# Optimization experiments

Hardware: AMD Instinct MI355X
Metric: run time of the kernel (lower is better)

## Reference

```python
import jax, jax.numpy as jnp
import numpy as np

B, T, D, K = 8, 2048, 256, 8192
COMMITMENT_COST = 0.25

def setup_inputs() -> dict:
    key = jax.random.key(0)
    k1, k2 = jax.random.split(key)
    xs = jax.random.normal(k1, (B, T, D), dtype=jnp.float32)
    # lengths: all full so max(ilens) == T and the wrapper slice is a no-op (static shapes for jit)
    ilens = jnp.full((B,), T, dtype=jnp.int64)
    codebook = jax.random.normal(k2, (K, D), dtype=jnp.float32)
    return {"xs": xs, "ilens": ilens, "codebook": codebook}

def reference(xs, ilens, codebook):
    # Quantizer.forward: slice xs to max(ilens) (no-op here, max(ilens)==T),
    # then VectorQuantize: euclidean nearest-codebook search + commitment loss.
    x_sq = jnp.sum(xs * xs, axis=-1, keepdims=True)              # (B, T, 1)
    c_sq = jnp.sum(codebook * codebook, axis=-1)                 # (K,)
    dots = jnp.einsum('btd,kd->btk', xs, codebook)               # (B, T, K)
    dist = x_sq - 2.0 * dots + c_sq                              # (B, T, K)
    indices = jnp.argmin(dist, axis=-1)                          # (B, T)
    quantized = codebook[indices]                                # (B, T, D) gather
    # commitment loss: mse(quantize.detach(), x)
    diff = jax.lax.stop_gradient(quantized) - xs
    commit_loss = jnp.mean(diff * diff)
    loss = COMMITMENT_COST * commit_loss
    return (loss, commit_loss)
```

## Files before the change

kernel.cpp:

```cpp
#include <hip/hip_runtime.h>
#include <stdint.h>

#define M_TOK 16384
#define DIM   256
#define KCB   8192
#define NGRP  8
#define GRP   1024
#define NCHK  16
#define NT    16
#define SHIFT 512.0f
#define INV_N (1.0f / 4194304.0f)
#define SC1   0x7F7F7F7F

typedef __attribute__((ext_vector_type(4))) float f32x4;
typedef __attribute__((ext_vector_type(8))) int   i32x8;

static __device__ __forceinline__ void lds_cp16(const void* g, void* l) {
    __builtin_amdgcn_global_load_lds(
        (const __attribute__((address_space(1))) void*)g,
        (__attribute__((address_space(3))) void*)l, 16, 0, 0);
}

static __device__ __forceinline__ int pk4(float4 f) {
    int o = __builtin_amdgcn_cvt_pk_fp8_f32(f.x, f.y, 0, false);
    o     = __builtin_amdgcn_cvt_pk_fp8_f32(f.z, f.w, o, true);
    return o;
}

__global__ void k_prep(const float* __restrict__ cb,
                       unsigned char* __restrict__ cbt,
                       float* __restrict__ chalf) {
    __shared__ float part[4][64];
    const int w  = threadIdx.x >> 6;
    const int l  = threadIdx.x & 63;
    const int c0 = blockIdx.x * 64;
    const float* row = cb + (size_t)(c0 + l) * DIM;
    float s = 0.0f;
    #pragma unroll
    for (int j = 0; j < 4; j++) {
        int ch = w * 4 + j;
        const float* p = row + ch * 16;
        float4 a = *(const float4*)(p);
        float4 b = *(const float4*)(p + 4);
        float4 c = *(const float4*)(p + 8);
        float4 d = *(const float4*)(p + 12);
        s += a.x*a.x + a.y*a.y + a.z*a.z + a.w*a.w
           + b.x*b.x + b.y*b.y + b.z*b.z + b.w*b.w
           + c.x*c.x + c.y*c.y + c.z*c.z + c.w*c.w
           + d.x*d.x + d.y*d.y + d.z*d.z + d.w*d.w;
        float4 na = {-a.x, -a.y, -a.z, -a.w};
        float4 nb = {-b.x, -b.y, -b.z, -b.w};
        float4 nc = {-c.x, -c.y, -c.z, -c.w};
        float4 nd = {-d.x, -d.y, -d.z, -d.w};
        uint4 r;
        r.x = (unsigned)pk4(na); r.y = (unsigned)pk4(nb);
        r.z = (unsigned)pk4(nc); r.w = (unsigned)pk4(nd);
        *(uint4*)(cbt + ((size_t)ch * KCB + c0 + l) * 16) = r;
    }
    part[w][l] = s;
    __syncthreads();
    if (w == 0) {
        float t = part[0][l] + part[1][l] + part[2][l] + part[3][l];
        chalf[c0 + l] = 0.5f * t + SHIFT;
    }
}

__global__ __launch_bounds__(256, 4) void k_gemm_argmin(
    const float* __restrict__ xs,
    const unsigned char* __restrict__ cbt,
    const float* __restrict__ chalf,
    uint32_t* __restrict__ pkey)
{
    __shared__ __align__(16) unsigned char Bs[2][NCHK][64][16];
    __shared__ float schalf[GRP];

    const int tid  = threadIdx.x;
    const int w    = tid >> 6;
    const int l    = tid & 63;
    const int lrow = l & 15;
    const int quad = l >> 4;
    const int m0 = blockIdx.x * 128;
    const int g  = blockIdx.y;

    *(float4*)&schalf[tid * 4] = ((const float4*)(chalf + g * GRP))[tid];

    const unsigned char* bsrc = cbt + ((size_t)(w * 4) * KCB + g * GRP + l) * 16;

    #pragma unroll
    for (int j = 0; j < 4; j++)
        lds_cp16(bsrc + (size_t)j * KCB * 16, &Bs[0][w * 4 + j][0][0]);

    i32x8 afr[2][2];
    {
        const float* ap = xs + (size_t)(m0 + w * 32 + lrow) * DIM + quad * 32;
        #pragma unroll
        for (int rt = 0; rt < 2; rt++)
            #pragma unroll
            for (int ks = 0; ks < 2; ks++) {
                const float* p = ap + rt * 16 * DIM + ks * 128;
                union { int d[8]; i32x8 v; } aa;
                #pragma unroll
                for (int d = 0; d < 8; d++)
                    aa.d[d] = pk4(*(const float4*)(p + d * 4));
                afr[rt][ks] = aa.v;
            }
    }

    uint32_t best[2][4];
    #pragma unroll
    for (int rt = 0; rt < 2; rt++)
        #pragma unroll
        for (int rg = 0; rg < 4; rg++) best[rt][rg] = 0xFFFFFFFFu;

    #pragma unroll 1
    for (int t = 0; t < NT; t++) {
        const int cur = t & 1;
        __syncthreads();
        if (t < NT - 1) {
            #pragma unroll
            for (int j = 0; j < 4; j++)
                lds_cp16(bsrc + ((size_t)j * KCB + (t + 1) * 64) * 16,
                         &Bs[1 - cur][w * 4 + j][0][0]);
        }

        f32x4 acc[2][4];
        #pragma unroll
        for (int ct = 0; ct < 4; ct++) {
            float cs = schalf[t * 64 + ct * 16 + lrow];
            #pragma unroll
            for (int rt = 0; rt < 2; rt++) {
                f32x4 c4 = {cs, cs, cs, cs};
                acc[rt][ct] = c4;
            }
        }
        #pragma unroll
        for (int ks = 0; ks < 2; ks++) {
            const int ch = ks * 8 + quad * 2;
            i32x8 bfr[4];
            #pragma unroll
            for (int ct = 0; ct < 4; ct++) {
                union { uint4 q[2]; i32x8 v; } bb;
                bb.q[0] = *(const uint4*)&Bs[cur][ch][ct * 16 + lrow][0];
                bb.q[1] = *(const uint4*)&Bs[cur][ch + 1][ct * 16 + lrow][0];
                bfr[ct] = bb.v;
            }
            #pragma unroll
            for (int rt = 0; rt < 2; rt++)
                #pragma unroll
                for (int ct = 0; ct < 4; ct++)
                    acc[rt][ct] = __builtin_amdgcn_mfma_scale_f32_16x16x128_f8f6f4(
                        afr[rt][ks], bfr[ct], acc[rt][ct],
                        0, 0,
                        0, SC1,
                        0, SC1);
        }
        #pragma unroll
        for (int ct = 0; ct < 4; ct++) {
            uint32_t idl = (uint32_t)(t * 64 + ct * 16 + lrow);
            #pragma unroll
            for (int rt = 0; rt < 2; rt++)
                #pragma unroll
                for (int rg = 0; rg < 4; rg++) {
                    uint32_t key =
                        (__float_as_uint(acc[rt][ct][rg]) & 0xFFFFFC00u) | idl;
                    if (key < best[rt][rg]) best[rt][rg] = key;
                }
        }
    }

    #pragma unroll
    for (int off = 1; off < 16; off <<= 1)
        #pragma unroll
        for (int rt = 0; rt < 2; rt++)
            #pragma unroll
            for (int rg = 0; rg < 4; rg++) {
                uint32_t o = __shfl_xor(best[rt][rg], off);
                if (o < best[rt][rg]) best[rt][rg] = o;
            }
    if (lrow == 0) {
        #pragma unroll
        for (int rt = 0; rt < 2; rt++)
            #pragma unroll
            for (int rg = 0; rg < 4; rg++)
                pkey[(size_t)(m0 + w * 32 + rt * 16 + quad * 4 + rg) * NGRP + g]
                    = best[rt][rg];
    }
}

__global__ void k_finalize(const uint32_t* __restrict__ pkey,
                           const float4* __restrict__ xs4,
                           const float4* __restrict__ cb4,
                           float* __restrict__ partial) {
    __shared__ float sblk[4];
    int w   = threadIdx.x >> 6;
    int row = blockIdx.x * 4 + w;
    int l   = threadIdx.x & 63;
    uint32_t k = 0xFFFFFFFFu;
    int g = 0;
    if (l < 8) { k = pkey[(size_t)row * NGRP + l]; g = l; }
    #pragma unroll
    for (int off = 1; off < 8; off <<= 1) {
        uint32_t ok = __shfl_xor(k, off);
        int      og = __shfl_xor(g, off);
        if (ok < k) { k = ok; g = og; }
    }
    k = __shfl(k, 0);
    g = __shfl(g, 0);
    int code = g * GRP + (int)(k & 1023u);
    float4 x = xs4[(size_t)row * 64 + l];
    float4 c = cb4[(size_t)code * 64 + l];
    float dx = x.x - c.x, dy = x.y - c.y, dz = x.z - c.z, dw = x.w - c.w;
    float s = dx * dx + dy * dy + dz * dz + dw * dw;
    #pragma unroll
    for (int off = 32; off; off >>= 1) s += __shfl_xor(s, off);
    if (l == 0) sblk[w] = s;
    __syncthreads();
    if (threadIdx.x == 0)
        partial[blockIdx.x] = sblk[0] + sblk[1] + sblk[2] + sblk[3];
}

__global__ void k_write(const float* __restrict__ partial,
                        float* __restrict__ out) {
    __shared__ float swv[16];
    int tid = threadIdx.x;
    float s = partial[tid] + partial[tid + 1024] +
              partial[tid + 2048] + partial[tid + 3072];
    #pragma unroll
    for (int off = 32; off; off >>= 1) s += __shfl_xor(s, off);
    if ((tid & 63) == 0) swv[tid >> 6] = s;
    __syncthreads();
    if (tid == 0) {
        float t = 0.0f;
        #pragma unroll
        for (int i = 0; i < 16; i++) t += swv[i];
        float commit = t * INV_N;
        out[0] = 0.25f * commit;
        out[1] = commit;
    }
}

extern "C" void kernel_launch(void* const* d_in, const int* in_sizes, int n_in,
                              void* d_out, int out_size, void* d_ws, size_t ws_size,
                              hipStream_t stream) {
    const float* xs = (const float*)d_in[0];
    const float* cb = (const float*)d_in[2];

    char* ws = (char*)d_ws;
    unsigned char* cbt     = (unsigned char*)(ws + 256);
    float*         chalf   = (float*)(ws + 256 + 2097152);
    uint32_t*      pkey    = (uint32_t*)(ws + 256 + 2129920);
    float*         partial = (float*)(ws + 256 + 2654208);

    k_prep<<<128, 256, 0, stream>>>(cb, cbt, chalf);
    dim3 g(M_TOK / 128, NGRP);
    k_gemm_argmin<<<g, 256, 0, stream>>>(xs, cbt, chalf, pkey);
    k_finalize<<<4096, 256, 0, stream>>>(pkey, (const float4*)xs,
                                         (const float4*)cb, partial);
    k_write<<<1, 1024, 0, stream>>>(partial, (float*)d_out);
}
```

Measured before the change: 119.6 us.

## Prefetch two stages ahead with explicit waitcnt and barrier scheduling in GEMM-argmin

The codebook tile pipeline in the fused GEMM/argmin kernel becomes prefetch-distance two. Two tiles are issued up front, and the loop uses explicit vmcnt waits, raw s_barrier and sched_barrier, and setprio around the MFMA bursts. The next load is issued mid-iteration, after the second k-slice's B fragments are read into registers, so the previous global load latency can overlap compute. The prep kernel is also split over twice as many blocks, each handling 32 codes, to raise parallelism. The hand-placed waitcnts are fragile and rely on the exact count of outstanding loads.

```diff
diff --git a/kernel.cpp b/kernel.cpp
--- a/kernel.cpp
+++ b/kernel.cpp
@@ -30,15 +30,18 @@
 __global__ void k_prep(const float* __restrict__ cb,
                        unsigned char* __restrict__ cbt,
                        float* __restrict__ chalf) {
-    __shared__ float part[4][64];
-    const int w  = threadIdx.x >> 6;
-    const int l  = threadIdx.x & 63;
-    const int c0 = blockIdx.x * 64;
-    const float* row = cb + (size_t)(c0 + l) * DIM;
+    __shared__ float part[8][32];
+    const int w    = threadIdx.x >> 6;
+    const int l    = threadIdx.x & 63;
+    const int code = l & 31;
+    const int sub  = l >> 5;
+    const int grp8 = w * 2 + sub;
+    const int c0   = blockIdx.x * 32;
+    const float* row = cb + (size_t)(c0 + code) * DIM;
     float s = 0.0f;
     #pragma unroll
-    for (int j = 0; j < 4; j++) {
-        int ch = w * 4 + j;
+    for (int j = 0; j < 2; j++) {
+        int ch = grp8 * 2 + j;
         const float* p = row + ch * 16;
         float4 a = *(const float4*)(p);
         float4 b = *(const float4*)(p + 4);
@@ -55,12 +58,14 @@
         uint4 r;
         r.x = (unsigned)pk4(na); r.y = (unsigned)pk4(nb);
         r.z = (unsigned)pk4(nc); r.w = (unsigned)pk4(nd);
-        *(uint4*)(cbt + ((size_t)ch * KCB + c0 + l) * 16) = r;
-    }
-    part[w][l] = s;
+        *(uint4*)(cbt + ((size_t)ch * KCB + c0 + code) * 16) = r;
+    }
+    part[grp8][code] = s;
     __syncthreads();
-    if (w == 0) {
-        float t = part[0][l] + part[1][l] + part[2][l] + part[3][l];
+    if (w == 0 && l < 32) {
+        float t = 0.0f;
+        #pragma unroll
+        for (int i = 0; i < 8; i++) t += part[i][l];
         chalf[c0 + l] = 0.5f * t + SHIFT;
     }
 }
@@ -82,13 +87,7 @@
     const int m0 = blockIdx.x * 128;
     const int g  = blockIdx.y;
 
-    *(float4*)&schalf[tid * 4] = ((const float4*)(chalf + g * GRP))[tid];
-
     const unsigned char* bsrc = cbt + ((size_t)(w * 4) * KCB + g * GRP + l) * 16;
-
-    #pragma unroll
-    for (int j = 0; j < 4; j++)
-        lds_cp16(bsrc + (size_t)j * KCB * 16, &Bs[0][w * 4 + j][0][0]);
 
     i32x8 afr[2][2];
     {
@@ -106,6 +105,16 @@
             }
     }
 
+    *(float4*)&schalf[tid * 4] = ((const float4*)(chalf + g * GRP))[tid];
+    asm volatile("s_waitcnt lgkmcnt(0)" ::: "memory");
+
+    #pragma unroll
+    for (int j = 0; j < 4; j++)
+        lds_cp16(bsrc + ((size_t)j * KCB + 0 * 64) * 16, &Bs[0][w * 4 + j][0][0]);
+    #pragma unroll
+    for (int j = 0; j < 4; j++)
+        lds_cp16(bsrc + ((size_t)j * KCB + 1 * 64) * 16, &Bs[1][w * 4 + j][0][0]);
+
     uint32_t best[2][4];
     #pragma unroll
     for (int rt = 0; rt < 2; rt++)
@@ -115,13 +124,10 @@
     #pragma unroll 1
     for (int t = 0; t < NT; t++) {
         const int cur = t & 1;
-        __syncthreads();
-        if (t < NT - 1) {
-            #pragma unroll
-            for (int j = 0; j < 4; j++)
-                lds_cp16(bsrc + ((size_t)j * KCB + (t + 1) * 64) * 16,
-                         &Bs[1 - cur][w * 4 + j][0][0]);
-        }
+        if (t == NT - 1) asm volatile("s_waitcnt vmcnt(0)" ::: "memory");
+        else             asm volatile("s_waitcnt vmcnt(4)" ::: "memory");
+        __builtin_amdgcn_s_barrier();
+        __builtin_amdgcn_sched_barrier(0);
 
         f32x4 acc[2][4];
         #pragma unroll
@@ -133,9 +139,9 @@
                 acc[rt][ct] = c4;
             }
         }
-        #pragma unroll
-        for (int ks = 0; ks < 2; ks++) {
-            const int ch = ks * 8 + quad * 2;
+
+        {
+            const int ch = quad * 2;
             i32x8 bfr[4];
             #pragma unroll
             for (int ct = 0; ct < 4; ct++) {
@@ -144,16 +150,50 @@
                 bb.q[1] = *(const uint4*)&Bs[cur][ch + 1][ct * 16 + lrow][0];
                 bfr[ct] = bb.v;
             }
+            __builtin_amdgcn_s_setprio(1);
             #pragma unroll
             for (int rt = 0; rt < 2; rt++)
                 #pragma unroll
                 for (int ct = 0; ct < 4; ct++)
                     acc[rt][ct] = __builtin_amdgcn_mfma_scale_f32_16x16x128_f8f6f4(
-                        afr[rt][ks], bfr[ct], acc[rt][ct],
-                        0, 0,
-                        0, SC1,
-                        0, SC1);
-        }
+                        afr[rt][0], bfr[ct], acc[rt][ct],
+                        0, 0, 0, SC1, 0, SC1);
+            __builtin_amdgcn_s_setprio(0);
+        }
+
+        i32x8 bfr1[4];
+        {
+            const int ch = 8 + quad * 2;
+            #pragma unroll
+            for (int ct = 0; ct < 4; ct++) {
+                union { uint4 q[2]; i32x8 v; } bb;
+                bb.q[0] = *(const uint4*)&Bs[cur][ch][ct * 16 + lrow][0];
+                bb.q[1] = *(const uint4*)&Bs[cur][ch + 1][ct * 16 + lrow][0];
+                bfr1[ct] = bb.v;
+            }
+        }
+        asm volatile("s_waitcnt lgkmcnt(0)" ::: "memory");
+        __builtin_amdgcn_sched_barrier(0);
+        __builtin_amdgcn_s_barrier();
+        __builtin_amdgcn_sched_barrier(0);
+
+        if (t < NT - 2) {
+            #pragma unroll
+            for (int j = 0; j < 4; j++)
+                lds_cp16(bsrc + ((size_t)j * KCB + (t + 2) * 64) * 16,
+                         &Bs[cur][w * 4 + j][0][0]);
+        }
+
+        __builtin_amdgcn_s_setprio(1);
+        #pragma unroll
+        for (int rt = 0; rt < 2; rt++)
+            #pragma unroll
+            for (int ct = 0; ct < 4; ct++)
+                acc[rt][ct] = __builtin_amdgcn_mfma_scale_f32_16x16x128_f8f6f4(
+                    afr[rt][1], bfr1[ct], acc[rt][ct],
+                    0, 0, 0, SC1, 0, SC1);
+        __builtin_amdgcn_s_setprio(0);
+
         #pragma unroll
         for (int ct = 0; ct < 4; ct++) {
             uint32_t idl = (uint32_t)(t * 64 + ct * 16 + lrow);
@@ -251,7 +291,7 @@
     uint32_t*      pkey    = (uint32_t*)(ws + 256 + 2129920);
     float*         partial = (float*)(ws + 256 + 2654208);
 
-    k_prep<<<128, 256, 0, stream>>>(cb, cbt, chalf);
+    k_prep<<<256, 256, 0, stream>>>(cb, cbt, chalf);
     dim3 g(M_TOK / 128, NGRP);
     k_gemm_argmin<<<g, 256, 0, stream>>>(xs, cbt, chalf, pkey);
     k_finalize<<<4096, 256, 0, stream>>>(pkey, (const float4*)xs,
```

After: 158.8 us. +32.9%, slower.

## Keep codebook fragments in registers and stream pre-quantized fp8 activations

Applied to the files above, without the earlier changes.

Before, each block held a 128-row activation tile in registers and streamed 1024 codes through LDS. Now each wave keeps a 64-code slice of the fp8 codebook in registers and streams 512 rows of activations, which k_prep pre-quantizes to fp8 in a chunked layout. Each wave reduces one 16-row step across its 64 codes, writing 128 partial keys per row instead of 8. k_finalize reduces those keys and also does the final sum via an atomic last-block counter, removing the separate k_write launch. The trade is many more partial-key writes and reads plus an extra activation quantization pass, in exchange for dropping LDS staging and barriers.

```diff
diff --git a/kernel.cpp b/kernel.cpp
--- a/kernel.cpp
+++ b/kernel.cpp
@@ -4,22 +4,14 @@
 #define M_TOK 16384
 #define DIM   256
 #define KCB   8192
-#define NGRP  8
-#define GRP   1024
-#define NCHK  16
-#define NT    16
+#define NCG   128
+#define NMS   32
 #define SHIFT 512.0f
 #define INV_N (1.0f / 4194304.0f)
 #define SC1   0x7F7F7F7F
 
 typedef __attribute__((ext_vector_type(4))) float f32x4;
 typedef __attribute__((ext_vector_type(8))) int   i32x8;
-
-static __device__ __forceinline__ void lds_cp16(const void* g, void* l) {
-    __builtin_amdgcn_global_load_lds(
-        (const __attribute__((address_space(1))) void*)g,
-        (__attribute__((address_space(3))) void*)l, 16, 0, 0);
-}
 
 static __device__ __forceinline__ int pk4(float4 f) {
     int o = __builtin_amdgcn_cvt_pk_fp8_f32(f.x, f.y, 0, false);
@@ -29,184 +21,191 @@
 
 __global__ void k_prep(const float* __restrict__ cb,
                        unsigned char* __restrict__ cbt,
-                       float* __restrict__ chalf) {
-    __shared__ float part[4][64];
-    const int w  = threadIdx.x >> 6;
-    const int l  = threadIdx.x & 63;
-    const int c0 = blockIdx.x * 64;
-    const float* row = cb + (size_t)(c0 + l) * DIM;
-    float s = 0.0f;
-    #pragma unroll
-    for (int j = 0; j < 4; j++) {
-        int ch = w * 4 + j;
-        const float* p = row + ch * 16;
-        float4 a = *(const float4*)(p);
-        float4 b = *(const float4*)(p + 4);
-        float4 c = *(const float4*)(p + 8);
-        float4 d = *(const float4*)(p + 12);
-        s += a.x*a.x + a.y*a.y + a.z*a.z + a.w*a.w
-           + b.x*b.x + b.y*b.y + b.z*b.z + b.w*b.w
-           + c.x*c.x + c.y*c.y + c.z*c.z + c.w*c.w
-           + d.x*d.x + d.y*d.y + d.z*d.z + d.w*d.w;
-        float4 na = {-a.x, -a.y, -a.z, -a.w};
-        float4 nb = {-b.x, -b.y, -b.z, -b.w};
-        float4 nc = {-c.x, -c.y, -c.z, -c.w};
-        float4 nd = {-d.x, -d.y, -d.z, -d.w};
-        uint4 r;
-        r.x = (unsigned)pk4(na); r.y = (unsigned)pk4(nb);
-        r.z = (unsigned)pk4(nc); r.w = (unsigned)pk4(nd);
-        *(uint4*)(cbt + ((size_t)ch * KCB + c0 + l) * 16) = r;
-    }
-    part[w][l] = s;
-    __syncthreads();
-    if (w == 0) {
-        float t = part[0][l] + part[1][l] + part[2][l] + part[3][l];
-        chalf[c0 + l] = 0.5f * t + SHIFT;
+                       float* __restrict__ chalf,
+                       const float* __restrict__ xs,
+                       unsigned char* __restrict__ xq,
+                       uint32_t* __restrict__ cnt) {
+    const int bid = blockIdx.x;
+    if (bid == 0 && threadIdx.x == 0) *cnt = 0;
+    const int w    = threadIdx.x >> 6;
+    const int l    = threadIdx.x & 63;
+    const int idx  = l & 31;
+    const int sub  = l >> 5;
+    const int grp8 = w * 2 + sub;
+
+    if (bid < 256) {
+        __shared__ float part[8][32];
+        const int c0 = bid * 32;
+        const float* row = cb + (size_t)(c0 + idx) * DIM;
+        float s = 0.0f;
+        #pragma unroll
+        for (int j = 0; j < 2; j++) {
+            int ch = grp8 * 2 + j;
+            const float* p = row + ch * 16;
+            float4 a = *(const float4*)(p);
+            float4 b = *(const float4*)(p + 4);
+            float4 c = *(const float4*)(p + 8);
+            float4 d = *(const float4*)(p + 12);
+            s += a.x*a.x + a.y*a.y + a.z*a.z + a.w*a.w
+               + b.x*b.x + b.y*b.y + b.z*b.z + b.w*b.w
+               + c.x*c.x + c.y*c.y + c.z*c.z + c.w*c.w
+               + d.x*d.x + d.y*d.y + d.z*d.z + d.w*d.w;
+            float4 na = {-a.x, -a.y, -a.z, -a.w};
+            float4 nb = {-b.x, -b.y, -b.z, -b.w};
+            float4 nc = {-c.x, -c.y, -c.z, -c.w};
+            float4 nd = {-d.x, -d.y, -d.z, -d.w};
+            uint4 r;
+            r.x = (unsigned)pk4(na); r.y = (unsigned)pk4(nb);
+            r.z = (unsigned)pk4(nc); r.w = (unsigned)pk4(nd);
+            *(uint4*)(cbt + ((size_t)ch * KCB + c0 + idx) * 16) = r;
+        }
+        part[grp8][idx] = s;
+        __syncthreads();
+        if (w == 0 && l < 32) {
+            float t = 0.0f;
+            #pragma unroll
+            for (int i = 0; i < 8; i++) t += part[i][l];
+            chalf[c0 + l] = 0.5f * t + SHIFT;
+        }
+    } else {
+        const int r0  = (bid - 256) * 32;
+        const float* row = xs + (size_t)(r0 + idx) * DIM;
+        #pragma unroll
+        for (int j = 0; j < 2; j++) {
+            int ch = grp8 * 2 + j;
+            const float* p = row + ch * 16;
+            uint4 r;
+            r.x = (unsigned)pk4(*(const float4*)(p));
+            r.y = (unsigned)pk4(*(const float4*)(p + 4));
+            r.z = (unsigned)pk4(*(const float4*)(p + 8));
+            r.w = (unsigned)pk4(*(const float4*)(p + 12));
+            *(uint4*)(xq + ((size_t)ch * M_TOK + r0 + idx) * 16) = r;
+        }
     }
 }
 
 __global__ __launch_bounds__(256, 4) void k_gemm_argmin(
-    const float* __restrict__ xs,
+    const unsigned char* __restrict__ xq,
     const unsigned char* __restrict__ cbt,
     const float* __restrict__ chalf,
     uint32_t* __restrict__ pkey)
 {
-    __shared__ __align__(16) unsigned char Bs[2][NCHK][64][16];
-    __shared__ float schalf[GRP];
-
     const int tid  = threadIdx.x;
     const int w    = tid >> 6;
     const int l    = tid & 63;
-    const int lrow = l & 15;
+    const int col  = l & 15;
     const int quad = l >> 4;
-    const int m0 = blockIdx.x * 128;
-    const int g  = blockIdx.y;
-
-    *(float4*)&schalf[tid * 4] = ((const float4*)(chalf + g * GRP))[tid];
-
-    const unsigned char* bsrc = cbt + ((size_t)(w * 4) * KCB + g * GRP + l) * 16;
-
-    #pragma unroll
-    for (int j = 0; j < 4; j++)
-        lds_cp16(bsrc + (size_t)j * KCB * 16, &Bs[0][w * 4 + j][0][0]);
-
-    i32x8 afr[2][2];
-    {
-        const float* ap = xs + (size_t)(m0 + w * 32 + lrow) * DIM + quad * 32;
-        #pragma unroll
-        for (int rt = 0; rt < 2; rt++)
-            #pragma unroll
-            for (int ks = 0; ks < 2; ks++) {
-                const float* p = ap + rt * 16 * DIM + ks * 128;
-                union { int d[8]; i32x8 v; } aa;
-                #pragma unroll
-                for (int d = 0; d < 8; d++)
-                    aa.d[d] = pk4(*(const float4*)(p + d * 4));
-                afr[rt][ks] = aa.v;
-            }
-    }
-
-    uint32_t best[2][4];
-    #pragma unroll
-    for (int rt = 0; rt < 2; rt++)
-        #pragma unroll
-        for (int rg = 0; rg < 4; rg++) best[rt][rg] = 0xFFFFFFFFu;
-
-    #pragma unroll 1
-    for (int t = 0; t < NT; t++) {
-        const int cur = t & 1;
-        __syncthreads();
-        if (t < NT - 1) {
-            #pragma unroll
-            for (int j = 0; j < 4; j++)
-                lds_cp16(bsrc + ((size_t)j * KCB + (t + 1) * 64) * 16,
-                         &Bs[1 - cur][w * 4 + j][0][0]);
-        }
-
-        f32x4 acc[2][4];
-        #pragma unroll
-        for (int ct = 0; ct < 4; ct++) {
-            float cs = schalf[t * 64 + ct * 16 + lrow];
-            #pragma unroll
-            for (int rt = 0; rt < 2; rt++) {
-                f32x4 c4 = {cs, cs, cs, cs};
-                acc[rt][ct] = c4;
-            }
-        }
+    const int bid  = blockIdx.x;
+    const int ms   = (bid & 7) * 4 + ((bid >> 3) & 3);
+    const int cg   = (bid >> 5) * 4 + w;
+    const int row0base = ms * 512;
+    const int chA = quad * 2, chB = 8 + quad * 2;
+    const uint32_t idbase = (uint32_t)((cg & 15) << 6);
+
+    i32x8 bfr[4][2];
+    #pragma unroll
+    for (int ct = 0; ct < 4; ct++) {
+        const int code = cg * 64 + ct * 16 + col;
         #pragma unroll
         for (int ks = 0; ks < 2; ks++) {
             const int ch = ks * 8 + quad * 2;
-            i32x8 bfr[4];
-            #pragma unroll
-            for (int ct = 0; ct < 4; ct++) {
-                union { uint4 q[2]; i32x8 v; } bb;
-                bb.q[0] = *(const uint4*)&Bs[cur][ch][ct * 16 + lrow][0];
-                bb.q[1] = *(const uint4*)&Bs[cur][ch + 1][ct * 16 + lrow][0];
-                bfr[ct] = bb.v;
-            }
-            #pragma unroll
-            for (int rt = 0; rt < 2; rt++)
-                #pragma unroll
-                for (int ct = 0; ct < 4; ct++)
-                    acc[rt][ct] = __builtin_amdgcn_mfma_scale_f32_16x16x128_f8f6f4(
-                        afr[rt][ks], bfr[ct], acc[rt][ct],
-                        0, 0,
-                        0, SC1,
-                        0, SC1);
-        }
-        #pragma unroll
-        for (int ct = 0; ct < 4; ct++) {
-            uint32_t idl = (uint32_t)(t * 64 + ct * 16 + lrow);
-            #pragma unroll
-            for (int rt = 0; rt < 2; rt++)
-                #pragma unroll
-                for (int rg = 0; rg < 4; rg++) {
-                    uint32_t key =
-                        (__float_as_uint(acc[rt][ct][rg]) & 0xFFFFFC00u) | idl;
-                    if (key < best[rt][rg]) best[rt][rg] = key;
-                }
-        }
-    }
-
-    #pragma unroll
-    for (int off = 1; off < 16; off <<= 1)
-        #pragma unroll
-        for (int rt = 0; rt < 2; rt++)
-            #pragma unroll
-            for (int rg = 0; rg < 4; rg++) {
-                uint32_t o = __shfl_xor(best[rt][rg], off);
-                if (o < best[rt][rg]) best[rt][rg] = o;
-            }
-    if (lrow == 0) {
-        #pragma unroll
-        for (int rt = 0; rt < 2; rt++)
-            #pragma unroll
-            for (int rg = 0; rg < 4; rg++)
-                pkey[(size_t)(m0 + w * 32 + rt * 16 + quad * 4 + rg) * NGRP + g]
-                    = best[rt][rg];
-    }
+            union { uint4 q[2]; i32x8 v; } bb;
+            bb.q[0] = *(const uint4*)(cbt + ((size_t)ch * KCB + code) * 16);
+            bb.q[1] = *(const uint4*)(cbt + ((size_t)(ch + 1) * KCB + code) * 16);
+            bfr[ct][ks] = bb.v;
+        }
+    }
+    float cs[4];
+    #pragma unroll
+    for (int ct = 0; ct < 4; ct++)
+        cs[ct] = chalf[cg * 64 + ct * 16 + col];
+
+#define ASTEP(S, C0a, C0b, N0a, N0b)                                          \
+    {                                                                         \
+        const int row0 = row0base + (S) * 16;                                 \
+        const size_t arow = (size_t)(row0 + col) * 16;                        \
+        uint4 A1a = *(const uint4*)(xq + (size_t)chB * (M_TOK * 16) + arow);  \
+        uint4 A1b = *(const uint4*)(xq + (size_t)(chB + 1) * (M_TOK * 16) + arow); \
+        union { uint4 q[2]; i32x8 v; } ua0; ua0.q[0] = C0a; ua0.q[1] = C0b;   \
+        f32x4 acc[4];                                                         \
+        _Pragma("unroll")                                                     \
+        for (int ct = 0; ct < 4; ct++) {                                      \
+            f32x4 c4 = {cs[ct], cs[ct], cs[ct], cs[ct]};                      \
+            acc[ct] = __builtin_amdgcn_mfma_scale_f32_16x16x128_f8f6f4(       \
+                ua0.v, bfr[ct][0], c4, 0, 0, 0, SC1, 0, SC1);                 \
+        }                                                                     \
+        const size_t nrow = (size_t)(row0base + (((S) + 1) & 31) * 16 + col) * 16; \
+        N0a = *(const uint4*)(xq + (size_t)chA * (M_TOK * 16) + nrow);        \
+        N0b = *(const uint4*)(xq + (size_t)(chA + 1) * (M_TOK * 16) + nrow);  \
+        union { uint4 q[2]; i32x8 v; } ua1; ua1.q[0] = A1a; ua1.q[1] = A1b;   \
+        _Pragma("unroll")                                                     \
+        for (int ct = 0; ct < 4; ct++)                                        \
+            acc[ct] = __builtin_amdgcn_mfma_scale_f32_16x16x128_f8f6f4(       \
+                ua1.v, bfr[ct][1], acc[ct], 0, 0, 0, SC1, 0, SC1);            \
+        uint32_t best4[4];                                                    \
+        _Pragma("unroll")                                                     \
+        for (int rg = 0; rg < 4; rg++) {                                      \
+            best4[rg] = (__float_as_uint(acc[0][rg]) & 0xFFFFFC00u)           \
+                        | (idbase + (uint32_t)col);                           \
+            _Pragma("unroll")                                                 \
+            for (int ct = 1; ct < 4; ct++) {                                  \
+                uint32_t key = (__float_as_uint(acc[ct][rg]) & 0xFFFFFC00u)   \
+                               | (idbase + (uint32_t)(ct * 16 + col));        \
+                if (key < best4[rg]) best4[rg] = key;                         \
+            }                                                                 \
+        }                                                                     \
+        _Pragma("unroll")                                                     \
+        for (int off = 1; off < 16; off <<= 1)                                \
+            _Pragma("unroll")                                                 \
+            for (int rg = 0; rg < 4; rg++) {                                  \
+                uint32_t o = __shfl_xor(best4[rg], off);                      \
+                if (o < best4[rg]) best4[rg] = o;                             \
+            }                                                                 \
+        if (col == 0) {                                                       \
+            _Pragma("unroll")                                                 \
+            for (int rg = 0; rg < 4; rg++)                                    \
+                pkey[(size_t)cg * M_TOK + row0 + quad * 4 + rg] = best4[rg];  \
+        }                                                                     \
+    }
+
+    uint4 A0a, A0b, N0a, N0b;
+    {
+        const size_t arow = (size_t)(row0base + col) * 16;
+        A0a = *(const uint4*)(xq + (size_t)chA * (M_TOK * 16) + arow);
+        A0b = *(const uint4*)(xq + (size_t)(chA + 1) * (M_TOK * 16) + arow);
+    }
+    #pragma unroll 1
+    for (int s = 0; s < 32; s += 2) {
+        ASTEP(s,     A0a, A0b, N0a, N0b)
+        ASTEP(s + 1, N0a, N0b, A0a, A0b)
+    }
+#undef ASTEP
 }
 
 __global__ void k_finalize(const uint32_t* __restrict__ pkey,
                            const float4* __restrict__ xs4,
                            const float4* __restrict__ cb4,
-                           float* __restrict__ partial) {
+                           float* __restrict__ partial,
+                           uint32_t* __restrict__ cnt,
+                           float* __restrict__ out) {
     __shared__ float sblk[4];
-    int w   = threadIdx.x >> 6;
-    int row = blockIdx.x * 4 + w;
-    int l   = threadIdx.x & 63;
-    uint32_t k = 0xFFFFFFFFu;
-    int g = 0;
-    if (l < 8) { k = pkey[(size_t)row * NGRP + l]; g = l; }
-    #pragma unroll
-    for (int off = 1; off < 8; off <<= 1) {
+    __shared__ int   last;
+    const int w   = threadIdx.x >> 6;
+    const int l   = threadIdx.x & 63;
+    const int row = blockIdx.x * 4 + w;
+
+    uint32_t k1 = pkey[(size_t)l * M_TOK + row];
+    uint32_t k2 = pkey[(size_t)(64 + l) * M_TOK + row];
+    uint32_t k;  int g;
+    if (k2 < k1) { k = k2; g = 64 + l; } else { k = k1; g = l; }
+    #pragma unroll
+    for (int off = 1; off < 64; off <<= 1) {
         uint32_t ok = __shfl_xor(k, off);
         int      og = __shfl_xor(g, off);
-        if (ok < k) { k = ok; g = og; }
-    }
-    k = __shfl(k, 0);
-    g = __shfl(g, 0);
-    int code = g * GRP + (int)(k & 1023u);
+        if (ok < k || (ok == k && og < g)) { k = ok; g = og; }
+    }
+    const int code = (g >> 4) * 1024 + (int)(k & 1023u);
+
     float4 x = xs4[(size_t)row * 64 + l];
     float4 c = cb4[(size_t)code * 64 + l];
     float dx = x.x - c.x, dy = x.y - c.y, dz = x.z - c.z, dw = x.w - c.w;
@@ -215,27 +214,28 @@
     for (int off = 32; off; off >>= 1) s += __shfl_xor(s, off);
     if (l == 0) sblk[w] = s;
     __syncthreads();
-    if (threadIdx.x == 0)
+    if (threadIdx.x == 0) {
         partial[blockIdx.x] = sblk[0] + sblk[1] + sblk[2] + sblk[3];
-}
-
-__global__ void k_write(const float* __restrict__ partial,
-                        float* __restrict__ out) {
-    __shared__ float swv[16];
-    int tid = threadIdx.x;
-    float s = partial[tid] + partial[tid + 1024] +
-              partial[tid + 2048] + partial[tid + 3072];
-    #pragma unroll
-    for (int off = 32; off; off >>= 1) s += __shfl_xor(s, off);
-    if ((tid & 63) == 0) swv[tid >> 6] = s;
+        __threadfence();
+        uint32_t old = atomicAdd(cnt, 1u);
+        last = (old == 4095u) ? 1 : 0;
+    }
     __syncthreads();
-    if (tid == 0) {
+    if (last) {
+        __threadfence();
         float t = 0.0f;
-        #pragma unroll
-        for (int i = 0; i < 16; i++) t += swv[i];
-        float commit = t * INV_N;
-        out[0] = 0.25f * commit;
-        out[1] = commit;
+        for (int i = threadIdx.x; i < 4096; i += 256) t += partial[i];
+        #pragma unroll
+        for (int off = 32; off; off >>= 1) t += __shfl_xor(t, off);
+        __syncthreads();
+        if (l == 0) sblk[w] = t;
+        __syncthreads();
+        if (threadIdx.x == 0) {
+            float tt = sblk[0] + sblk[1] + sblk[2] + sblk[3];
+            float commit = tt * INV_N;
+            out[0] = 0.25f * commit;
+            out[1] = commit;
+        }
     }
 }
 
@@ -246,15 +246,16 @@
     const float* cb = (const float*)d_in[2];
 
     char* ws = (char*)d_ws;
-    unsigned char* cbt     = (unsigned char*)(ws + 256);
-    float*         chalf   = (float*)(ws + 256 + 2097152);
-    uint32_t*      pkey    = (uint32_t*)(ws + 256 + 2129920);
-    float*         partial = (float*)(ws + 256 + 2654208);
-
-    k_prep<<<128, 256, 0, stream>>>(cb, cbt, chalf);
-    dim3 g(M_TOK / 128, NGRP);
-    k_gemm_argmin<<<g, 256, 0, stream>>>(xs, cbt, chalf, pkey);
+    uint32_t*      cnt     = (uint32_t*)(ws);
+    float*         partial = (float*)(ws + 256);
+    float*         chalf   = (float*)(ws + 16640);
+    unsigned char* cbt     = (unsigned char*)(ws + 49408);
+    unsigned char* xq      = (unsigned char*)(ws + 2146560);
+    uint32_t*      pkey    = (uint32_t*)(ws + 6340864);
+
+    k_prep<<<768, 256, 0, stream>>>(cb, cbt, chalf, xs, xq, cnt);
+    k_gemm_argmin<<<1024, 256, 0, stream>>>(xq, cbt, chalf, pkey);
     k_finalize<<<4096, 256, 0, stream>>>(pkey, (const float4*)xs,
-                                         (const float4*)cb, partial);
-    k_write<<<1, 1024, 0, stream>>>(partial, (float*)d_out);
-}
+                                         (const float4*)cb, partial, cnt,
+                                         (float*)d_out);
+}
```

Measured after the change: 254.7 us. +113.1%, slower.
